# Kernel optimization log

Measured on AMD Instinct MI355X. Metric: run time of the kernel, lower is better.

## Reference

```python
import jax, jax.numpy as jnp
import numpy as np
from jax import lax

EPS = 1e-5  # BatchNorm eps (inference-style BN with running stats)


def _bn(x, g, b, m, v):
    scale = g / jnp.sqrt(v + EPS)
    return x * scale[None, :, None, None] + (b - m * scale)[None, :, None, None]


def _conv1x1_bn(x, w, g, b, m, v):
    # ConvNormActivation(in_ch, out, k=1, activation=None) -> 1x1 conv (no bias) + BN
    y = jnp.einsum('bchw,oc->bohw', x, w)
    return _bn(y, g, b, m, v)


def _upsample_bilinear_ac(x, scale):
    # nn.Upsample(scale_factor=scale, mode='bilinear', align_corners=True)
    B, C, H, W = x.shape
    Ho, Wo = H * scale, W * scale

    def coords(n_in, n_out):
        s = jnp.arange(n_out, dtype=x.dtype) * ((n_in - 1) / (n_out - 1))
        i0 = jnp.clip(jnp.floor(s).astype(jnp.int32), 0, n_in - 2)
        t = s - i0.astype(x.dtype)
        return i0, t

    iy, ty = coords(H, Ho)
    ix, tx = coords(W, Wo)
    x = x[:, :, iy, :] * (1 - ty)[None, None, :, None] + x[:, :, iy + 1, :] * ty[None, None, :, None]
    x = x[:, :, :, ix] * (1 - tx) + x[:, :, :, ix + 1] * tx
    return x


def _dcnv2(x, off_w, off_b, w):
    # DCNv2: internal 3x3 conv -> 18 offsets (dy,dx per tap) + 9 sigmoid masks,
    # then modulated deformable 3x3 conv (stride 1, pad 1, no bias).
    B, C, H, W = x.shape
    K2 = 9
    om = lax.conv_general_dilated(x, off_w, (1, 1), ((1, 1), (1, 1)),
                                  dimension_numbers=('NCHW', 'OIHW', 'NCHW'))
    om = om + off_b[None, :, None, None]
    off = om[:, :2 * K2].reshape(B, K2, 2, H, W)          # (dy, dx) per kernel tap
    mask = jax.nn.sigmoid(om[:, 2 * K2:3 * K2])           # [B,9,H,W]

    ky, kx = jnp.meshgrid(jnp.arange(3), jnp.arange(3), indexing='ij')
    base_y = (jnp.arange(H)[None, :, None] + (ky.reshape(K2) - 1)[:, None, None]).astype(x.dtype)  # [9,H,1]
    base_x = (jnp.arange(W)[None, None, :] + (kx.reshape(K2) - 1)[:, None, None]).astype(x.dtype)  # [9,1,W]
    sy = base_y[None] + off[:, :, 0]                      # [B,9,H,W]
    sx = base_x[None] + off[:, :, 1]

    xf = x.reshape(B, C, H * W)
    y0 = jnp.floor(sy)
    x0 = jnp.floor(sx)
    val = jnp.zeros((B, C, K2, H, W), x.dtype)
    for dy in (0, 1):
        for dx in (0, 1):
            yy = y0 + dy
            xx = x0 + dx
            wgt = (1 - jnp.abs(sy - yy)) * (1 - jnp.abs(sx - xx))
            valid = (yy >= 0) & (yy <= H - 1) & (xx >= 0) & (xx <= W - 1)
            idx = jnp.clip(yy, 0, H - 1).astype(jnp.int32) * W + jnp.clip(xx, 0, W - 1).astype(jnp.int32)
            g = jnp.take_along_axis(xf, idx.reshape(B, 1, -1), axis=2).reshape(B, C, K2, H, W)
            val = val + g * (wgt * valid.astype(x.dtype))[:, None]
    val = val * mask[:, None]
    return jnp.einsum('bckhw,ock->bohw', val, w.reshape(w.shape[0], C, K2))


def _forward(f0, f1, f2, f3,
             w0, g0, b0, m0, v0, w1, g1, b1, m1, v1,
             w2, g2, b2, m2, v2, w3, g3, b3, m3, v3,
             off_w, off_b, dcn_w, gf, bf, mf, vf):
    x1 = _conv1x1_bn(f0, w0, g0, b0, m0, v0)
    x2 = _upsample_bilinear_ac(_conv1x1_bn(f1, w1, g1, b1, m1, v1), 2)
    x3 = _upsample_bilinear_ac(_conv1x1_bn(f2, w2, g2, b2, m2, v2), 4)
    x4 = _upsample_bilinear_ac(_conv1x1_bn(f3, w3, g3, b3, m3, v3), 8)
    x = jax.nn.relu(x1 + x2 + x3 + x4)
    y = _dcnv2(x, off_w, off_b, dcn_w)
    return jax.nn.relu(_bn(y, gf, bf, mf, vf))


def setup_inputs() -> dict:
    key = jax.random.key(0)
    ks = iter(jax.random.split(key, 64))

    def rn(shape, scale=1.0):
        return jax.random.normal(next(ks), shape, dtype=jnp.float32) * scale

    def ru(shape):
        return jax.random.uniform(next(ks), shape, dtype=jnp.float32)

    C = 64
    inp = {}
    inp['f0'] = rn((4, 64, 160, 160))
    inp['f1'] = rn((4, 128, 80, 80))
    inp['f2'] = rn((4, 256, 40, 40))
    inp['f3'] = rn((4, 512, 20, 20))
    for i, cin in enumerate([64, 128, 256, 512]):
        inp[f'w{i}'] = rn((C, cin), 1.0 / np.sqrt(cin))
        inp[f'g{i}'] = rn((C,))
        inp[f'b{i}'] = rn((C,))
        inp[f'm{i}'] = rn((C,))
        inp[f'v{i}'] = ru((C,))
    inp['off_w'] = rn((27, C, 3, 3), 0.01)   # small offsets, like post-training DCN
    inp['off_b'] = rn((27,), 0.01)
    inp['dcn_w'] = rn((C, C, 3, 3), 1.0 / np.sqrt(C * 9))
    inp['gf'] = rn((C,))
    inp['bf'] = rn((C,))
    inp['mf'] = rn((C,))
    inp['vf'] = ru((C,))
    return inp


def reference(f0, f1, f2, f3,
              w0, g0, b0, m0, v0, w1, g1, b1, m1, v1,
              w2, g2, b2, m2, v2, w3, g3, b3, m3, v3,
              off_w, off_b, dcn_w, gf, bf, mf, vf):
    return _forward(f0, f1, f2, f3,
                    w0, g0, b0, m0, v0, w1, g1, b1, m1, v1,
                    w2, g2, b2, m2, v2, w3, g3, b3, m3, v3,
                    off_w, off_b, dcn_w, gf, bf, mf, vf)
```

## Files before the change

kernel.cpp:

```cpp
#include <hip/hip_runtime.h>
#include <math.h>

#define EPSB 1e-5f

constexpr int B_ = 4;
constexpr int C_ = 64;
constexpr int H_ = 160;
constexpr int W_ = 160;
constexpr int HW_ = H_ * W_;

constexpr size_t X_OFF   = 0;
constexpr size_t Y1_OFF  = X_OFF  + (size_t)B_ * HW_ * 64;
constexpr size_t Y2_OFF  = Y1_OFF + (size_t)B_ * 6400 * 64;
constexpr size_t Y3_OFF  = Y2_OFF + (size_t)B_ * 1600 * 64;
constexpr size_t OM_OFF  = Y3_OFF + (size_t)B_ * 400 * 64;
constexpr size_t WR0_OFF = OM_OFF + (size_t)B_ * HW_ * 27;
constexpr size_t WTB_OFF = WR0_OFF + 4096;
constexpr size_t RWB_OFF = WTB_OFF + (9 * 64 * 72) / 2;
constexpr size_t SB_OFF  = RWB_OFF + (9 * 32 * 64) / 2;
constexpr size_t WR1_OFF = X_OFF + 0;
constexpr size_t WR2_OFF = X_OFF + 8192;
constexpr size_t WR3_OFF = X_OFF + 24576;

typedef short bf16x8 __attribute__((ext_vector_type(8)));
typedef float f32x4 __attribute__((ext_vector_type(4)));
typedef unsigned int u32x2 __attribute__((ext_vector_type(2)));

static __device__ __forceinline__ unsigned short f2bf(float f) {
    unsigned int u = __float_as_uint(f);
    u += 0x7fff + ((u >> 16) & 1);
    return (unsigned short)(u >> 16);
}

__global__ __launch_bounds__(256) void prep_kernel(
    const float* __restrict__ g0, const float* __restrict__ b0, const float* __restrict__ m0, const float* __restrict__ v0,
    const float* __restrict__ g1, const float* __restrict__ b1, const float* __restrict__ m1, const float* __restrict__ v1,
    const float* __restrict__ g2, const float* __restrict__ b2, const float* __restrict__ m2, const float* __restrict__ v2,
    const float* __restrict__ g3, const float* __restrict__ b3, const float* __restrict__ m3, const float* __restrict__ v3,
    const float* __restrict__ gf, const float* __restrict__ bf, const float* __restrict__ mf, const float* __restrict__ vf,
    const float* __restrict__ w0, const float* __restrict__ w1, const float* __restrict__ w2, const float* __restrict__ w3,
    const float* __restrict__ dcn_w, const float* __restrict__ off_w,
    float* __restrict__ ws)
{
    int tid = blockIdx.x * 256 + threadIdx.x;
    if (tid < 320) {
        int j = tid >> 6, c = tid & 63;
        const float *g, *b, *m, *v;
        switch (j) {
            case 0: g = g0; b = b0; m = m0; v = v0; break;
            case 1: g = g1; b = b1; m = m1; v = v1; break;
            case 2: g = g2; b = b2; m = m2; v = v2; break;
            case 3: g = g3; b = b3; m = m3; v = v3; break;
            default: g = gf; b = bf; m = mf; v = vf; break;
        }
        float sc = g[c] * rsqrtf(v[c] + EPSB);
        ws[SB_OFF + j * 128 + c]      = sc;
        ws[SB_OFF + j * 128 + 64 + c] = b[c] - m[c] * sc;
        return;
    }
    int t = tid - 320;
    if (t < 4096) {
        int ci = t >> 6, o = t & 63;
        ws[WR0_OFF + t] = w0[o * 64 + ci];
        return;
    }
    t -= 4096;
    if (t < 9 * 64 * 72) {
        int k = t / 4608, r = t % 4608, o = r / 72, c = r % 72;
        float v = (c < 64) ? dcn_w[o * 576 + c * 9 + k] : 0.f;
        ((unsigned short*)(ws + WTB_OFF))[t] = f2bf(v);
        return;
    }
    t -= 9 * 64 * 72;
    if (t < 9 * 32 * 64) {
        int tap = t >> 11, r = t & 2047, o = r >> 6, ci = r & 63;
        float v = (o < 27) ? off_w[o * 576 + ci * 9 + tap] : 0.f;
        ((unsigned short*)(ws + RWB_OFF))[t] = f2bf(v);
        return;
    }
    t -= 9 * 32 * 64;
    if (t < 8192) {
        int ci = t >> 6, o = t & 63;
        ws[WR1_OFF + t] = w1[o * 128 + ci];
        return;
    }
    t -= 8192;
    if (t < 16384) {
        int ci = t >> 6, o = t & 63;
        ws[WR2_OFF + t] = w2[o * 256 + ci];
        return;
    }
    t -= 16384;
    if (t < 32768) {
        int ci = t >> 6, o = t & 63;
        ws[WR3_OFF + t] = w3[o * 512 + ci];
        return;
    }
}

__global__ __launch_bounds__(256) void conv_all_kernel(
    const float* __restrict__ f1in, const float* __restrict__ f2in, const float* __restrict__ f3in,
    float* __restrict__ ws)
{
    __shared__ float R0[64 * 65];
    __shared__ float R1[64 * 65];
    __shared__ float SBl[128];

    int blk = blockIdx.x;
    const float* fin; const float* wr; const float* sbg; float* yout;
    int Cin, hw, tile;
    if (blk < 400)      { fin = f1in; wr = ws + WR1_OFF; sbg = ws + SB_OFF + 128; yout = ws + Y1_OFF; Cin = 128; hw = 6400; tile = blk; }
    else if (blk < 500) { fin = f2in; wr = ws + WR2_OFF; sbg = ws + SB_OFF + 256; yout = ws + Y2_OFF; Cin = 256; hw = 1600; tile = blk - 400; }
    else                { fin = f3in; wr = ws + WR3_OFF; sbg = ws + SB_OFF + 384; yout = ws + Y3_OFF; Cin = 512; hw = 400;  tile = blk - 500; }

    int tid  = threadIdx.x;
    int lane = tid & 63;
    int wv   = __builtin_amdgcn_readfirstlane(tid >> 6);

    if (tid < 128) SBl[tid] = sbg[tid];

    int P = tile * 64 + lane;
    int b = P / hw;
    int p = P - b * hw;

    int cq = Cin >> 2;
    const float* fb = fin + ((size_t)b * Cin + (size_t)wv * cq) * hw + p;
    const float* wq = wr + (wv * cq) * 64;

    float acc[64];
#pragma unroll
    for (int o = 0; o < 64; o++) acc[o] = 0.f;

    for (int c0 = 0; c0 < cq; c0 += 16) {
        float fv[16];
#pragma unroll
        for (int j = 0; j < 16; j++) fv[j] = fb[(size_t)(c0 + j) * hw];
#pragma unroll
        for (int j = 0; j < 16; j++) {
            const float* wrow = wq + (c0 + j) * 64;
#pragma unroll
            for (int o = 0; o < 64; o++) acc[o] = fmaf(fv[j], wrow[o], acc[o]);
        }
    }

    if (wv == 2) {
#pragma unroll
        for (int o = 0; o < 64; o++) R0[lane * 65 + o] = acc[o];
    }
    if (wv == 3) {
#pragma unroll
        for (int o = 0; o < 64; o++) R1[lane * 65 + o] = acc[o];
    }
    __syncthreads();
    if (wv == 0) {
#pragma unroll
        for (int o = 0; o < 64; o++) acc[o] += R0[lane * 65 + o];
    }
    if (wv == 1) {
#pragma unroll
        for (int o = 0; o < 64; o++) acc[o] += R1[lane * 65 + o];
    }
    __syncthreads();
    if (wv == 1) {
#pragma unroll
        for (int o = 0; o < 64; o++) R0[lane * 65 + o] = acc[o];
    }
    __syncthreads();
    if (wv == 0) {
#pragma unroll
        for (int o = 0; o < 64; o++) {
            float v = acc[o] + R0[lane * 65 + o];
            R1[lane * 65 + o] = fmaf(v, SBl[o], SBl[64 + o]);
        }
    }
    __syncthreads();

#pragma unroll
    for (int it = 0; it < 16; it++) {
        int idx = it * 256 + tid;
        int px = idx >> 6, o = idx & 63;
        yout[(size_t)(tile * 64 + px) * 64 + o] = R1[px * 65 + o];
    }
}

__global__ __launch_bounds__(256) void fuse_kernel(const float* __restrict__ f0, float* __restrict__ ws)
{
    __shared__ float Ot[64 * 68];

    int tid = threadIdx.x;
    int blk = blockIdx.x;
    int xcd = blk & 7, slot = blk >> 3;
    int b = xcd >> 1;
    int t = (xcd & 1) * 200 + slot;
    int p0 = t * 64;
    int lane = tid & 63;
    int cb = __builtin_amdgcn_readfirstlane(tid >> 6);
    int p = p0 + lane;
    const float* wr0 = ws + WR0_OFF + cb * 16;
    const float* sb  = ws + SB_OFF;

    {
        float acc[16];
#pragma unroll
        for (int i = 0; i < 16; i++) acc[i] = 0.f;

        const float* f0b = f0 + (size_t)b * 64 * HW_ + p;
        for (int ci0 = 0; ci0 < 64; ci0 += 16) {
            float fv[16];
#pragma unroll
            for (int j = 0; j < 16; j++) fv[j] = f0b[(size_t)(ci0 + j) * HW_];
#pragma unroll
            for (int j = 0; j < 16; j++) {
                const float* wrow = wr0 + (ci0 + j) * 64;
#pragma unroll
                for (int i = 0; i < 16; i++) acc[i] = fmaf(fv[j], wrow[i], acc[i]);
            }
        }
        float* orow = Ot + lane * 68 + cb * 16;
#pragma unroll
        for (int i = 0; i < 16; i++) {
            int o = cb * 16 + i;
            orow[i] = fmaf(acc[i], sb[o], sb[64 + o]);
        }
    }
    __syncthreads();

    {
        int chunk = lane & 15, pxo = lane >> 4;
        unsigned short* xb = (unsigned short*)(ws + X_OFF) + ((size_t)b * HW_ + p0) * 64;
#pragma unroll
        for (int r = 0; r < 4; r++) {
            int gpx = cb * 16 + r * 4 + pxo;
            int gp = p0 + gpx;
            int h = gp / W_, w = gp % W_;

            float fy1 = h * (79.f / 159.f); int i1 = (int)fy1; if (i1 > 78) i1 = 78; float ty1 = fy1 - i1;
            float fx1 = w * (79.f / 159.f); int j1 = (int)fx1; if (j1 > 78) j1 = 78; float tx1 = fx1 - j1;
            const float* y1 = ws + Y1_OFF + ((size_t)b * 6400 + (size_t)(i1 * 80 + j1)) * 64 + chunk * 4;
            float fy2 = h * (39.f / 159.f); int i2 = (int)fy2; if (i2 > 38) i2 = 38; float ty2 = fy2 - i2;
            float fx2 = w * (39.f / 159.f); int j2 = (int)fx2; if (j2 > 38) j2 = 38; float tx2 = fx2 - j2;
            const float* y2 = ws + Y2_OFF + ((size_t)b * 1600 + (size_t)(i2 * 40 + j2)) * 64 + chunk * 4;
            float fy3 = h * (19.f / 159.f); int i3 = (int)fy3; if (i3 > 18) i3 = 18; float ty3 = fy3 - i3;
            float fx3 = w * (19.f / 159.f); int j3 = (int)fx3; if (j3 > 18) j3 = 18; float tx3 = fx3 - j3;
            const float* y3 = ws + Y3_OFF + ((size_t)b * 400 + (size_t)(i3 * 20 + j3)) * 64 + chunk * 4;

            f32x4 A[12];
            A[0]  = *(const f32x4*)(y1);
            A[1]  = *(const f32x4*)(y1 + 64);
            A[2]  = *(const f32x4*)(y1 + 80 * 64);
            A[3]  = *(const f32x4*)(y1 + 81 * 64);
            A[4]  = *(const f32x4*)(y2);
            A[5]  = *(const f32x4*)(y2 + 64);
            A[6]  = *(const f32x4*)(y2 + 40 * 64);
            A[7]  = *(const f32x4*)(y2 + 41 * 64);
            A[8]  = *(const f32x4*)(y3);
            A[9]  = *(const f32x4*)(y3 + 64);
            A[10] = *(const f32x4*)(y3 + 20 * 64);
            A[11] = *(const f32x4*)(y3 + 21 * 64);

            f32x4 v = *(const f32x4*)(Ot + gpx * 68 + chunk * 4);

            float w00, w01, w10, w11;
            w00 = (1.f - ty1) * (1.f - tx1); w01 = (1.f - ty1) * tx1; w10 = ty1 * (1.f - tx1); w11 = ty1 * tx1;
#pragma unroll
            for (int j = 0; j < 4; j++)
                v[j] += A[0][j] * w00 + A[1][j] * w01 + A[2][j] * w10 + A[3][j] * w11;
            w00 = (1.f - ty2) * (1.f - tx2); w01 = (1.f - ty2) * tx2; w10 = ty2 * (1.f - tx2); w11 = ty2 * tx2;
#pragma unroll
            for (int j = 0; j < 4; j++)
                v[j] += A[4][j] * w00 + A[5][j] * w01 + A[6][j] * w10 + A[7][j] * w11;
            w00 = (1.f - ty3) * (1.f - tx3); w01 = (1.f - ty3) * tx3; w10 = ty3 * (1.f - tx3); w11 = ty3 * tx3;
#pragma unroll
            for (int j = 0; j < 4; j++)
                v[j] += A[8][j] * w00 + A[9][j] * w01 + A[10][j] * w10 + A[11][j] * w11;

#pragma unroll
            for (int j = 0; j < 4; j++) v[j] = fmaxf(v[j], 0.f);
            unsigned int lo = ((unsigned int)f2bf(v[1]) << 16) | f2bf(v[0]);
            unsigned int hi = ((unsigned int)f2bf(v[3]) << 16) | f2bf(v[2]);
            *(u32x2*)(xb + (size_t)gpx * 64 + chunk * 4) = (u32x2){lo, hi};
        }
    }
}

__global__ __launch_bounds__(256, 6) void dcn_fused_kernel(const float* __restrict__ off_b,
                                                           float* __restrict__ ws, float* __restrict__ out)
{
    __shared__ __align__(16) unsigned short A_lds[2][64 * 72];
    __shared__ float OMs[64 * 27];

    int tid = threadIdx.x;
    int blk = blockIdx.x;
    int xcd = blk & 7, slot = blk >> 3;
    int b = xcd >> 1;
    int t = (xcd & 1) * 200 + slot;
    int p0 = t * 64;
    int lane = tid & 63, cb = tid >> 6;
    int px = lane;
    int p = p0 + px;
    int h = p / W_, w = p % W_;
    int mrow = lane & 15, quad = lane >> 4;
    int chunk = lane & 15, pxo = lane >> 4;

    const unsigned short* rwb = (const unsigned short*)(ws + RWB_OFF);
    const unsigned short* wtb = (const unsigned short*)(ws + WTB_OFF);
    const unsigned short* xbh = (const unsigned short*)(ws + X_OFF) + (size_t)b * HW_ * 64;
    const float* sb = ws + SB_OFF + 4 * 128;

    {
        f32x4 acc2[2];
        acc2[0] = (f32x4){0.f, 0.f, 0.f, 0.f};
        acc2[1] = (f32x4){0.f, 0.f, 0.f, 0.f};

        for (int kk = 0; kk < 9; kk += 2) {
#pragma unroll
            for (int u = 0; u < 2; u++) {
                int tap = kk + u;
                if (tap > 8) break;
                int dy = tap / 3 - 1, dx = tap % 3 - 1;
                int delta = dy * W_ + dx;
                int  pss[4];
                bool vlds[4];
#pragma unroll
                for (int r = 0; r < 4; r++) {
                    int gpx = cb * 16 + r * 4 + pxo;
                    int gp = p0 + gpx;
                    int gh = gp / W_, gw = gp % W_;
                    int yy = gh + dy, xx = gw + dx;
                    vlds[r] = (yy >= 0) && (yy < H_) && (xx >= 0) && (xx < W_);
                    int ps = gp + delta;
                    pss[r] = min(max(ps, 0), HW_ - 1);
                }
                u32x2 g[4];
#pragma unroll
                for (int r = 0; r < 4; r++)
                    g[r] = *(const u32x2*)(xbh + (size_t)pss[r] * 64 + chunk * 4);
#pragma unroll
                for (int r = 0; r < 4; r++) {
                    int gpx = cb * 16 + r * 4 + pxo;
                    u32x2 gv;
                    gv.x = vlds[r] ? g[r].x : 0u;
                    gv.y = vlds[r] ? g[r].y : 0u;
                    *(u32x2*)(A_lds[u] + gpx * 72 + chunk * 4) = gv;
                }
            }

#pragma unroll
            for (int u = 0; u < 2; u++) {
                int tap = kk + u;
                if (tap > 8) break;
                const unsigned short* Ab = A_lds[u] + (cb * 16 + mrow) * 72;
#pragma unroll
                for (int ks = 0; ks < 2; ks++) {
                    bf16x8 af = *(const bf16x8*)(Ab + ks * 32 + quad * 8);
#pragma unroll
                    for (int nt = 0; nt < 2; nt++) {
                        bf16x8 bf_ = *(const bf16x8*)(rwb + tap * 2048 + (nt * 16 + mrow) * 64 + ks * 32 + quad * 8);
                        acc2[nt] = __builtin_amdgcn_mfma_f32_16x16x32_bf16(af, bf_, acc2[nt], 0, 0, 0);
                    }
                }
            }
        }

        __syncthreads();
        float* Cl = (float*)A_lds;
#pragma unroll
        for (int nt = 0; nt < 2; nt++) {
            int o = nt * 16 + mrow;
            if (o < 27) {
                int pr = cb * 16 + quad * 4;
#pragma unroll
                for (int r = 0; r < 4; r++) Cl[(pr + r) * 28 + o] = acc2[nt][r];
            }
        }
        __syncthreads();

        for (int k = cb; k < 9; k += 4) {
            float ady = Cl[px * 28 + 2 * k]     + off_b[2 * k];
            float adx = Cl[px * 28 + 2 * k + 1] + off_b[2 * k + 1];
            float am  = Cl[px * 28 + 18 + k]    + off_b[18 + k];
            float sy = (float)(h + k / 3 - 1) + ady;
            float sx = (float)(w + k % 3 - 1) + adx;
            float mk = 1.f / (1.f + __expf(-am));
            OMs[px * 27 + 3 * k]     = sy;
            OMs[px * 27 + 3 * k + 1] = sx;
            OMs[px * 27 + 3 * k + 2] = mk;
        }
        __syncthreads();
    }

    f32x4 acc[4];
#pragma unroll
    for (int nt = 0; nt < 4; nt++) acc[nt] = (f32x4){0.f, 0.f, 0.f, 0.f};

    for (int kk = 0; kk < 9; kk += 2) {
#pragma unroll
        for (int u = 0; u < 2; u++) {
            int k = kk + u;
            if (k > 8) break;
#pragma unroll
            for (int rp = 0; rp < 2; rp++) {
                int   idxs[2][4];
                float wvs[2][4];
#pragma unroll
                for (int rr = 0; rr < 2; rr++) {
                    int r = rp * 2 + rr;
                    int gpx = cb * 16 + r * 4 + pxo;
                    float sy = OMs[gpx * 27 + 3 * k];
                    float sx = OMs[gpx * 27 + 3 * k + 1];
                    float mk = OMs[gpx * 27 + 3 * k + 2];
                    float y0f = floorf(sy), x0f = floorf(sx);
                    int y0 = (int)y0f, x0 = (int)x0f;
                    float ty = sy - y0f, tx = sx - x0f;
#pragma unroll
                    for (int cr = 0; cr < 4; cr++) {
                        int dy = cr >> 1, dx = cr & 1;
                        int yy = y0 + dy, xx = x0 + dx;
                        float wy = dy ? ty : 1.f - ty;
                        float wx = dx ? tx : 1.f - tx;
                        bool vld = (yy >= 0) && (yy < H_) && (xx >= 0) && (xx < W_);
                        int yc = min(max(yy, 0), H_ - 1);
                        int xc = min(max(xx, 0), W_ - 1);
                        idxs[rr][cr] = yc * W_ + xc;
                        wvs[rr][cr]  = vld ? wy * wx * mk : 0.f;
                    }
                }
                u32x2 g[2][4];
#pragma unroll
                for (int rr = 0; rr < 2; rr++)
#pragma unroll
                    for (int cr = 0; cr < 4; cr++)
                        g[rr][cr] = *(const u32x2*)(xbh + (size_t)idxs[rr][cr] * 64 + chunk * 4);
#pragma unroll
                for (int rr = 0; rr < 2; rr++) {
                    int r = rp * 2 + rr;
                    int gpx = cb * 16 + r * 4 + pxo;
                    f32x4 v = (f32x4){0.f, 0.f, 0.f, 0.f};
#pragma unroll
                    for (int cr = 0; cr < 4; cr++) {
                        float wv = wvs[rr][cr];
                        float e0 = __uint_as_float(g[rr][cr].x << 16);
                        float e1 = __uint_as_float(g[rr][cr].x & 0xffff0000u);
                        float e2 = __uint_as_float(g[rr][cr].y << 16);
                        float e3 = __uint_as_float(g[rr][cr].y & 0xffff0000u);
                        v[0] = fmaf(e0, wv, v[0]);
                        v[1] = fmaf(e1, wv, v[1]);
                        v[2] = fmaf(e2, wv, v[2]);
                        v[3] = fmaf(e3, wv, v[3]);
                    }
                    unsigned int lo = ((unsigned int)f2bf(v[1]) << 16) | f2bf(v[0]);
                    unsigned int hi = ((unsigned int)f2bf(v[3]) << 16) | f2bf(v[2]);
                    *(u32x2*)(A_lds[u] + gpx * 72 + chunk * 4) = (u32x2){lo, hi};
                }
            }
        }

#pragma unroll
        for (int u = 0; u < 2; u++) {
            int k = kk + u;
            if (k > 8) break;
            const unsigned short* Ab = A_lds[u] + (cb * 16 + mrow) * 72;
#pragma unroll
            for (int ks = 0; ks < 2; ks++) {
                bf16x8 af = *(const bf16x8*)(Ab + ks * 32 + quad * 8);
#pragma unroll
                for (int nt = 0; nt < 4; nt++) {
                    bf16x8 bf_ = *(const bf16x8*)(wtb + k * 4608 + (nt * 16 + mrow) * 72 + ks * 32 + quad * 8);
                    acc[nt] = __builtin_amdgcn_mfma_f32_16x16x32_bf16(af, bf_, acc[nt], 0, 0, 0);
                }
            }
        }
    }

    __syncthreads();
    float* C_lds = (float*)A_lds;
#pragma unroll
    for (int nt = 0; nt < 4; nt++) {
        int o = nt * 16 + mrow;
        int pxb = cb * 16 + quad * 4;
#pragma unroll
        for (int r = 0; r < 4; r++) C_lds[o * 65 + pxb + r] = acc[nt][r];
    }
    __syncthreads();
#pragma unroll
    for (int i = 0; i < 16; i++) {
        int o = cb * 16 + i;
        float v = C_lds[o * 65 + lane];
        v = fmaf(v, sb[o], sb[64 + o]);
        out[((size_t)b * 64 + o) * HW_ + p0 + lane] = fmaxf(v, 0.f);
    }
}

extern "C" void kernel_launch(void* const* d_in, const int* in_sizes, int n_in,
                              void* d_out, int out_size, void* d_ws, size_t ws_size,
                              hipStream_t stream)
{
    const float* f0 = (const float*)d_in[0];
    const float* f1 = (const float*)d_in[1];
    const float* f2 = (const float*)d_in[2];
    const float* f3 = (const float*)d_in[3];
    const float* w0 = (const float*)d_in[4];
    const float* g0 = (const float*)d_in[5];
    const float* b0 = (const float*)d_in[6];
    const float* m0 = (const float*)d_in[7];
    const float* v0 = (const float*)d_in[8];
    const float* w1 = (const float*)d_in[9];
    const float* g1 = (const float*)d_in[10];
    const float* b1 = (const float*)d_in[11];
    const float* m1 = (const float*)d_in[12];
    const float* v1 = (const float*)d_in[13];
    const float* w2 = (const float*)d_in[14];
    const float* g2 = (const float*)d_in[15];
    const float* b2 = (const float*)d_in[16];
    const float* m2 = (const float*)d_in[17];
    const float* v2 = (const float*)d_in[18];
    const float* w3 = (const float*)d_in[19];
    const float* g3 = (const float*)d_in[20];
    const float* b3 = (const float*)d_in[21];
    const float* m3 = (const float*)d_in[22];
    const float* v3 = (const float*)d_in[23];
    const float* off_w = (const float*)d_in[24];
    const float* off_b = (const float*)d_in[25];
    const float* dcn_w = (const float*)d_in[26];
    const float* gf = (const float*)d_in[27];
    const float* bf = (const float*)d_in[28];
    const float* mf = (const float*)d_in[29];
    const float* vf = (const float*)d_in[30];

    float* ws  = (float*)d_ws;
    float* out = (float*)d_out;

    prep_kernel<<<dim3(476), dim3(256), 0, stream>>>(
        g0, b0, m0, v0, g1, b1, m1, v1, g2, b2, m2, v2, g3, b3, m3, v3,
        gf, bf, mf, vf, w0, w1, w2, w3, dcn_w, off_w, ws);

    conv_all_kernel<<<dim3(525), dim3(256), 0, stream>>>(f1, f2, f3, ws);

    fuse_kernel<<<dim3(1600), dim3(256), 0, stream>>>(f0, ws);

    dcn_fused_kernel<<<dim3(1600), dim3(256), 0, stream>>>(off_b, ws, out);
}
```

Measured before the change: 291.9 us.

## Restructure 1x1 convs to 4 pixels per thread with output-channel split across waves

Both the lateral 1x1 conv kernel and the fuse kernel now have each thread handle 4 contiguous pixels with float4 loads, and each wave owns 16 output channels instead of splitting input channels. This removes the LDS cross-wave reduction and its barriers in the conv kernel and raises arithmetic reuse per weight load. The fuse kernel also keeps its intermediate tile in LDS as bf16, and both kernels launch far fewer blocks (132 and 400). The risks are low occupancy and poor load balance from so few blocks, the loss of the XCD-aware block mapping, and extra rounding from the bf16 intermediate.

```diff
diff --git a/kernel.cpp b/kernel.cpp
--- a/kernel.cpp
+++ b/kernel.cpp
@@ -4,7 +4,6 @@
 #define EPSB 1e-5f
 
 constexpr int B_ = 4;
-constexpr int C_ = 64;
 constexpr int H_ = 160;
 constexpr int W_ = 160;
 constexpr int HW_ = H_ * W_;
@@ -30,6 +29,9 @@
     unsigned int u = __float_as_uint(f);
     u += 0x7fff + ((u >> 16) & 1);
     return (unsigned short)(u >> 16);
+}
+static __device__ __forceinline__ float bf2f(unsigned short s) {
+    return __uint_as_float((unsigned int)s << 16);
 }
 
 __global__ __launch_bounds__(256) void prep_kernel(
@@ -98,141 +100,127 @@
     }
 }
 
-__global__ __launch_bounds__(256) void conv_all_kernel(
+__global__ __launch_bounds__(256) void conv_v2_kernel(
     const float* __restrict__ f1in, const float* __restrict__ f2in, const float* __restrict__ f3in,
     float* __restrict__ ws)
 {
-    __shared__ float R0[64 * 65];
-    __shared__ float R1[64 * 65];
-    __shared__ float SBl[128];
-
     int blk = blockIdx.x;
     const float* fin; const float* wr; const float* sbg; float* yout;
     int Cin, hw, tile;
-    if (blk < 400)      { fin = f1in; wr = ws + WR1_OFF; sbg = ws + SB_OFF + 128; yout = ws + Y1_OFF; Cin = 128; hw = 6400; tile = blk; }
-    else if (blk < 500) { fin = f2in; wr = ws + WR2_OFF; sbg = ws + SB_OFF + 256; yout = ws + Y2_OFF; Cin = 256; hw = 1600; tile = blk - 400; }
-    else                { fin = f3in; wr = ws + WR3_OFF; sbg = ws + SB_OFF + 384; yout = ws + Y3_OFF; Cin = 512; hw = 400;  tile = blk - 500; }
+    if (blk < 100)      { fin = f1in; wr = ws + WR1_OFF; sbg = ws + SB_OFF + 128; yout = ws + Y1_OFF; Cin = 128; hw = 6400; tile = blk; }
+    else if (blk < 125) { fin = f2in; wr = ws + WR2_OFF; sbg = ws + SB_OFF + 256; yout = ws + Y2_OFF; Cin = 256; hw = 1600; tile = blk - 100; }
+    else                { fin = f3in; wr = ws + WR3_OFF; sbg = ws + SB_OFF + 384; yout = ws + Y3_OFF; Cin = 512; hw = 400;  tile = blk - 125; }
 
     int tid  = threadIdx.x;
     int lane = tid & 63;
     int wv   = __builtin_amdgcn_readfirstlane(tid >> 6);
 
-    if (tid < 128) SBl[tid] = sbg[tid];
-
-    int P = tile * 64 + lane;
-    int b = P / hw;
-    int p = P - b * hw;
-
-    int cq = Cin >> 2;
-    const float* fb = fin + ((size_t)b * Cin + (size_t)wv * cq) * hw + p;
-    const float* wq = wr + (wv * cq) * 64;
-
-    float acc[64];
-#pragma unroll
-    for (int o = 0; o < 64; o++) acc[o] = 0.f;
-
-    for (int c0 = 0; c0 < cq; c0 += 16) {
-        float fv[16];
-#pragma unroll
-        for (int j = 0; j < 16; j++) fv[j] = fb[(size_t)(c0 + j) * hw];
+    int gp = tile * 256 + lane * 4;
+    if (gp >= B_ * hw) return;
+    int b = gp / hw;
+    int p = gp - b * hw;
+
+    const float* fb = fin + (size_t)b * Cin * hw + p;
+    const float* wq = wr + 16 * wv;
+
+    f32x4 acc[16];
+#pragma unroll
+    for (int i = 0; i < 16; i++) acc[i] = (f32x4){0.f, 0.f, 0.f, 0.f};
+
+    for (int c0 = 0; c0 < Cin; c0 += 16) {
+        f32x4 fv[16];
+#pragma unroll
+        for (int j = 0; j < 16; j++) fv[j] = *(const f32x4*)(fb + (size_t)(c0 + j) * hw);
 #pragma unroll
         for (int j = 0; j < 16; j++) {
             const float* wrow = wq + (c0 + j) * 64;
 #pragma unroll
-            for (int o = 0; o < 64; o++) acc[o] = fmaf(fv[j], wrow[o], acc[o]);
-        }
-    }
-
-    if (wv == 2) {
-#pragma unroll
-        for (int o = 0; o < 64; o++) R0[lane * 65 + o] = acc[o];
-    }
-    if (wv == 3) {
-#pragma unroll
-        for (int o = 0; o < 64; o++) R1[lane * 65 + o] = acc[o];
+            for (int i = 0; i < 16; i++) {
+                float wval = wrow[i];
+#pragma unroll
+                for (int q = 0; q < 4; q++) acc[i][q] = fmaf(fv[j][q], wval, acc[i][q]);
+            }
+        }
+    }
+
+    float sc[16], bi[16];
+#pragma unroll
+    for (int i = 0; i < 16; i++) { sc[i] = sbg[16 * wv + i]; bi[i] = sbg[64 + 16 * wv + i]; }
+
+#pragma unroll
+    for (int q = 0; q < 4; q++) {
+        float ov[16];
+#pragma unroll
+        for (int i = 0; i < 16; i++) ov[i] = fmaf(acc[i][q], sc[i], bi[i]);
+#pragma unroll
+        for (int i2 = 0; i2 < 4; i2++) {
+            f32x4 st = {ov[4 * i2], ov[4 * i2 + 1], ov[4 * i2 + 2], ov[4 * i2 + 3]};
+            *(f32x4*)(yout + (size_t)(gp + q) * 64 + 16 * wv + 4 * i2) = st;
+        }
+    }
+}
+
+__global__ __launch_bounds__(256) void fuse_v2_kernel(const float* __restrict__ f0, float* __restrict__ ws)
+{
+    __shared__ unsigned short Ot[256 * 66];
+
+    int tid  = threadIdx.x;
+    int blk  = blockIdx.x;
+    int lane = tid & 63;
+    int wv   = __builtin_amdgcn_readfirstlane(tid >> 6);
+
+    int P0 = blk * 256;
+    int b  = __builtin_amdgcn_readfirstlane(P0 / HW_);
+    int pl0 = P0 - b * HW_;
+
+    {
+        const float* f0b = f0 + (size_t)b * 64 * HW_ + pl0 + lane * 4;
+        const float* wq  = ws + WR0_OFF + 16 * wv;
+
+        f32x4 acc[16];
+#pragma unroll
+        for (int i = 0; i < 16; i++) acc[i] = (f32x4){0.f, 0.f, 0.f, 0.f};
+
+        for (int c0 = 0; c0 < 64; c0 += 16) {
+            f32x4 fv[16];
+#pragma unroll
+            for (int j = 0; j < 16; j++) fv[j] = *(const f32x4*)(f0b + (size_t)(c0 + j) * HW_);
+#pragma unroll
+            for (int j = 0; j < 16; j++) {
+                const float* wrow = wq + (c0 + j) * 64;
+#pragma unroll
+                for (int i = 0; i < 16; i++) {
+                    float wval = wrow[i];
+#pragma unroll
+                    for (int q = 0; q < 4; q++) acc[i][q] = fmaf(fv[j][q], wval, acc[i][q]);
+                }
+            }
+        }
+        const float* sb = ws + SB_OFF;
+#pragma unroll
+        for (int q = 0; q < 4; q++) {
+            int px = lane * 4 + q;
+            unsigned short* orow = Ot + px * 66 + 16 * wv;
+#pragma unroll
+            for (int i = 0; i < 16; i += 2) {
+                float v0 = fmaf(acc[i][q],     sb[16 * wv + i],     sb[64 + 16 * wv + i]);
+                float v1 = fmaf(acc[i + 1][q], sb[16 * wv + i + 1], sb[64 + 16 * wv + i + 1]);
+                *(unsigned int*)(orow + i) = ((unsigned int)f2bf(v1) << 16) | f2bf(v0);
+            }
+        }
     }
     __syncthreads();
-    if (wv == 0) {
-#pragma unroll
-        for (int o = 0; o < 64; o++) acc[o] += R0[lane * 65 + o];
-    }
-    if (wv == 1) {
-#pragma unroll
-        for (int o = 0; o < 64; o++) acc[o] += R1[lane * 65 + o];
-    }
-    __syncthreads();
-    if (wv == 1) {
-#pragma unroll
-        for (int o = 0; o < 64; o++) R0[lane * 65 + o] = acc[o];
-    }
-    __syncthreads();
-    if (wv == 0) {
-#pragma unroll
-        for (int o = 0; o < 64; o++) {
-            float v = acc[o] + R0[lane * 65 + o];
-            R1[lane * 65 + o] = fmaf(v, SBl[o], SBl[64 + o]);
-        }
-    }
-    __syncthreads();
-
-#pragma unroll
-    for (int it = 0; it < 16; it++) {
-        int idx = it * 256 + tid;
-        int px = idx >> 6, o = idx & 63;
-        yout[(size_t)(tile * 64 + px) * 64 + o] = R1[px * 65 + o];
-    }
-}
-
-__global__ __launch_bounds__(256) void fuse_kernel(const float* __restrict__ f0, float* __restrict__ ws)
-{
-    __shared__ float Ot[64 * 68];
-
-    int tid = threadIdx.x;
-    int blk = blockIdx.x;
-    int xcd = blk & 7, slot = blk >> 3;
-    int b = xcd >> 1;
-    int t = (xcd & 1) * 200 + slot;
-    int p0 = t * 64;
-    int lane = tid & 63;
-    int cb = __builtin_amdgcn_readfirstlane(tid >> 6);
-    int p = p0 + lane;
-    const float* wr0 = ws + WR0_OFF + cb * 16;
-    const float* sb  = ws + SB_OFF;
 
     {
-        float acc[16];
-#pragma unroll
-        for (int i = 0; i < 16; i++) acc[i] = 0.f;
-
-        const float* f0b = f0 + (size_t)b * 64 * HW_ + p;
-        for (int ci0 = 0; ci0 < 64; ci0 += 16) {
-            float fv[16];
-#pragma unroll
-            for (int j = 0; j < 16; j++) fv[j] = f0b[(size_t)(ci0 + j) * HW_];
-#pragma unroll
-            for (int j = 0; j < 16; j++) {
-                const float* wrow = wr0 + (ci0 + j) * 64;
-#pragma unroll
-                for (int i = 0; i < 16; i++) acc[i] = fmaf(fv[j], wrow[i], acc[i]);
-            }
-        }
-        float* orow = Ot + lane * 68 + cb * 16;
-#pragma unroll
-        for (int i = 0; i < 16; i++) {
-            int o = cb * 16 + i;
-            orow[i] = fmaf(acc[i], sb[o], sb[64 + o]);
-        }
-    }
-    __syncthreads();
-
-    {
-        int chunk = lane & 15, pxo = lane >> 4;
-        unsigned short* xb = (unsigned short*)(ws + X_OFF) + ((size_t)b * HW_ + p0) * 64;
-#pragma unroll
-        for (int r = 0; r < 4; r++) {
-            int gpx = cb * 16 + r * 4 + pxo;
-            int gp = p0 + gpx;
-            int h = gp / W_, w = gp % W_;
+        int chunk = tid & 15;
+        int pxb   = tid >> 4;
+        unsigned short* xws = (unsigned short*)(ws + X_OFF);
+
+        for (int it = 0; it < 16; it++) {
+            int px = pxb + it * 16;
+            int pl = pl0 + px;
+            int gp = P0 + px;
+            int h = pl / W_, w = pl % W_;
 
             float fy1 = h * (79.f / 159.f); int i1 = (int)fy1; if (i1 > 78) i1 = 78; float ty1 = fy1 - i1;
             float fx1 = w * (79.f / 159.f); int j1 = (int)fx1; if (j1 > 78) j1 = 78; float tx1 = fx1 - j1;
@@ -258,7 +246,12 @@
             A[10] = *(const f32x4*)(y3 + 20 * 64);
             A[11] = *(const f32x4*)(y3 + 21 * 64);
 
-            f32x4 v = *(const f32x4*)(Ot + gpx * 68 + chunk * 4);
+            u32x2 ov = *(const u32x2*)(Ot + px * 66 + chunk * 4);
+            f32x4 v;
+            v[0] = bf2f((unsigned short)(ov.x & 0xffff));
+            v[1] = bf2f((unsigned short)(ov.x >> 16));
+            v[2] = bf2f((unsigned short)(ov.y & 0xffff));
+            v[3] = bf2f((unsigned short)(ov.y >> 16));
 
             float w00, w01, w10, w11;
             w00 = (1.f - ty1) * (1.f - tx1); w01 = (1.f - ty1) * tx1; w10 = ty1 * (1.f - tx1); w11 = ty1 * tx1;
@@ -278,7 +271,7 @@
             for (int j = 0; j < 4; j++) v[j] = fmaxf(v[j], 0.f);
             unsigned int lo = ((unsigned int)f2bf(v[1]) << 16) | f2bf(v[0]);
             unsigned int hi = ((unsigned int)f2bf(v[3]) << 16) | f2bf(v[2]);
-            *(u32x2*)(xb + (size_t)gpx * 64 + chunk * 4) = (u32x2){lo, hi};
+            *(u32x2*)(xws + (size_t)gp * 64 + chunk * 4) = (u32x2){lo, hi};
         }
     }
 }
@@ -534,9 +527,9 @@
         g0, b0, m0, v0, g1, b1, m1, v1, g2, b2, m2, v2, g3, b3, m3, v3,
         gf, bf, mf, vf, w0, w1, w2, w3, dcn_w, off_w, ws);
 
-    conv_all_kernel<<<dim3(525), dim3(256), 0, stream>>>(f1, f2, f3, ws);
-
-    fuse_kernel<<<dim3(1600), dim3(256), 0, stream>>>(f0, ws);
+    conv_v2_kernel<<<dim3(132), dim3(256), 0, stream>>>(f1, f2, f3, ws);
+
+    fuse_v2_kernel<<<dim3(400), dim3(256), 0, stream>>>(f0, ws);
 
     dcn_fused_kernel<<<dim3(1600), dim3(256), 0, stream>>>(off_b, ws, out);
 }
```

New measurement: 390.8 us. +33.9%, slower.

## Split conv work by output channels per wave with 4 pixels per lane

Applied to the files above, without the earlier changes.

The 1x1 conv kernel for the three lower-resolution feature maps stops splitting the input-channel reduction across waves. Each wave now computes 16 of the 64 output channels over the full input-channel range, and each lane handles 4 consecutive pixels using vector loads. This removes the shared-memory reduction, the barriers and the transposed store stage, and writes outputs directly with vector stores. The grid shrinks from 525 to 132 blocks, which leaves fewer blocks to fill the GPU. The kernel relies on f32x4 being defined elsewhere in the file.

```diff
diff --git a/kernel.cpp b/kernel.cpp
--- a/kernel.cpp
+++ b/kernel.cpp
@@ -4,7 +4,6 @@
 #define EPSB 1e-5f
 
 constexpr int B_ = 4;
-constexpr int C_ = 64;
 constexpr int H_ = 160;
 constexpr int W_ = 160;
 constexpr int HW_ = H_ * W_;
@@ -98,88 +97,63 @@
     }
 }
 
-__global__ __launch_bounds__(256) void conv_all_kernel(
+__global__ __launch_bounds__(256, 1) void conv_v3_kernel(
     const float* __restrict__ f1in, const float* __restrict__ f2in, const float* __restrict__ f3in,
     float* __restrict__ ws)
 {
-    __shared__ float R0[64 * 65];
-    __shared__ float R1[64 * 65];
-    __shared__ float SBl[128];
-
     int blk = blockIdx.x;
     const float* fin; const float* wr; const float* sbg; float* yout;
     int Cin, hw, tile;
-    if (blk < 400)      { fin = f1in; wr = ws + WR1_OFF; sbg = ws + SB_OFF + 128; yout = ws + Y1_OFF; Cin = 128; hw = 6400; tile = blk; }
-    else if (blk < 500) { fin = f2in; wr = ws + WR2_OFF; sbg = ws + SB_OFF + 256; yout = ws + Y2_OFF; Cin = 256; hw = 1600; tile = blk - 400; }
-    else                { fin = f3in; wr = ws + WR3_OFF; sbg = ws + SB_OFF + 384; yout = ws + Y3_OFF; Cin = 512; hw = 400;  tile = blk - 500; }
+    if (blk < 100)      { fin = f1in; wr = ws + WR1_OFF; sbg = ws + SB_OFF + 128; yout = ws + Y1_OFF; Cin = 128; hw = 6400; tile = blk; }
+    else if (blk < 125) { fin = f2in; wr = ws + WR2_OFF; sbg = ws + SB_OFF + 256; yout = ws + Y2_OFF; Cin = 256; hw = 1600; tile = blk - 100; }
+    else                { fin = f3in; wr = ws + WR3_OFF; sbg = ws + SB_OFF + 384; yout = ws + Y3_OFF; Cin = 512; hw = 400;  tile = blk - 125; }
 
     int tid  = threadIdx.x;
     int lane = tid & 63;
     int wv   = __builtin_amdgcn_readfirstlane(tid >> 6);
 
-    if (tid < 128) SBl[tid] = sbg[tid];
-
-    int P = tile * 64 + lane;
-    int b = P / hw;
-    int p = P - b * hw;
-
-    int cq = Cin >> 2;
-    const float* fb = fin + ((size_t)b * Cin + (size_t)wv * cq) * hw + p;
-    const float* wq = wr + (wv * cq) * 64;
-
-    float acc[64];
-#pragma unroll
-    for (int o = 0; o < 64; o++) acc[o] = 0.f;
-
-    for (int c0 = 0; c0 < cq; c0 += 16) {
-        float fv[16];
-#pragma unroll
-        for (int j = 0; j < 16; j++) fv[j] = fb[(size_t)(c0 + j) * hw];
+    int gp = tile * 256 + lane * 4;
+    if (gp >= B_ * hw) return;
+    int b = gp / hw;
+    int p = gp - b * hw;
+
+    const float* fb = fin + (size_t)b * Cin * hw + p;
+    const float* wq = wr + 16 * wv;
+
+    f32x4 acc[16];
+#pragma unroll
+    for (int i = 0; i < 16; i++) acc[i] = (f32x4){0.f, 0.f, 0.f, 0.f};
+
+    for (int c0 = 0; c0 < Cin; c0 += 16) {
+        f32x4 fv[16];
+#pragma unroll
+        for (int j = 0; j < 16; j++) fv[j] = *(const f32x4*)(fb + (size_t)(c0 + j) * hw);
 #pragma unroll
         for (int j = 0; j < 16; j++) {
             const float* wrow = wq + (c0 + j) * 64;
 #pragma unroll
-            for (int o = 0; o < 64; o++) acc[o] = fmaf(fv[j], wrow[o], acc[o]);
-        }
-    }
-
-    if (wv == 2) {
-#pragma unroll
-        for (int o = 0; o < 64; o++) R0[lane * 65 + o] = acc[o];
-    }
-    if (wv == 3) {
-#pragma unroll
-        for (int o = 0; o < 64; o++) R1[lane * 65 + o] = acc[o];
-    }
-    __syncthreads();
-    if (wv == 0) {
-#pragma unroll
-        for (int o = 0; o < 64; o++) acc[o] += R0[lane * 65 + o];
-    }
-    if (wv == 1) {
-#pragma unroll
-        for (int o = 0; o < 64; o++) acc[o] += R1[lane * 65 + o];
-    }
-    __syncthreads();
-    if (wv == 1) {
-#pragma unroll
-        for (int o = 0; o < 64; o++) R0[lane * 65 + o] = acc[o];
-    }
-    __syncthreads();
-    if (wv == 0) {
-#pragma unroll
-        for (int o = 0; o < 64; o++) {
-            float v = acc[o] + R0[lane * 65 + o];
-            R1[lane * 65 + o] = fmaf(v, SBl[o], SBl[64 + o]);
-        }
-    }
-    __syncthreads();
-
-#pragma unroll
-    for (int it = 0; it < 16; it++) {
-        int idx = it * 256 + tid;
-        int px = idx >> 6, o = idx & 63;
-        yout[(size_t)(tile * 64 + px) * 64 + o] = R1[px * 65 + o];
+            for (int i = 0; i < 16; i++) {
+                float wval = wrow[i];
+#pragma unroll
+                for (int q = 0; q < 4; q++) acc[i][q] = fmaf(fv[j][q], wval, acc[i][q]);
+            }
+        }
+    }
+
+    float sc[16], bi[16];
+#pragma unroll
+    for (int i = 0; i < 16; i++) { sc[i] = sbg[16 * wv + i]; bi[i] = sbg[64 + 16 * wv + i]; }
+
+#pragma unroll
+    for (int q = 0; q < 4; q++) {
+        float ov[16];
+#pragma unroll
+        for (int i = 0; i < 16; i++) ov[i] = fmaf(acc[i][q], sc[i], bi[i]);
+#pragma unroll
+        for (int i2 = 0; i2 < 4; i2++) {
+            f32x4 st = {ov[4 * i2], ov[4 * i2 + 1], ov[4 * i2 + 2], ov[4 * i2 + 3]};
+            *(f32x4*)(yout + (size_t)(gp + q) * 64 + 16 * wv + 4 * i2) = st;
+        }
     }
 }
 
@@ -534,7 +508,7 @@
         g0, b0, m0, v0, g1, b1, m1, v1, g2, b2, m2, v2, g3, b3, m3, v3,
         gf, bf, mf, vf, w0, w1, w2, w3, dcn_w, off_w, ws);
 
-    conv_all_kernel<<<dim3(525), dim3(256), 0, stream>>>(f1, f2, f3, ws);
+    conv_v3_kernel<<<dim3(132), dim3(256), 0, stream>>>(f1, f2, f3, ws);
 
     fuse_kernel<<<dim3(1600), dim3(256), 0, stream>>>(f0, ws);
 
```

New measurement: 380.8 us. 30.5% more time.
